# Kernel tuning notes

Hardware: AMD Instinct MI355X
Metric: run time of the kernel (lower is better)

The kernel has to match this reference:

```python
import jax, jax.numpy as jnp
import numpy as np

BATCH = 16384
NUM_CLASSES = 1000
FEA_DIM = 1024
MARGIN = 5.0


def setup_inputs() -> dict:
    key = jax.random.key(0)
    k1, k2, k3 = jax.random.split(key, 3)
    x = jax.random.normal(k1, (BATCH, FEA_DIM), dtype=jnp.float32)
    labels = jax.random.randint(k2, (BATCH,), 0, NUM_CLASSES)
    centers = jax.random.normal(k3, (NUM_CLASSES, FEA_DIM), dtype=jnp.float32)
    return {"x": x, "labels": labels, "centers": centers}


def reference(x, labels, centers):
    # Half squared euclidean distances via the GEMM expansion:
    # 0.5*||a-b||^2 = 0.5*(||a||^2 + ||b||^2 - 2 a.b)
    B = x.shape[0]
    C = centers.shape[0]
    x2 = jnp.sum(x * x, axis=1, keepdims=True)          # [B,1]
    c2 = jnp.sum(centers * centers, axis=1)             # [C]
    d_xc = 0.5 * (x2 + c2[None, :] - 2.0 * (x @ centers.T))   # [B,C]
    d_cc = 0.5 * (c2[:, None] + c2[None, :] - 2.0 * (centers @ centers.T))  # [C,C]

    is_label = labels[:, None] == jnp.arange(C)[None, :]  # [B,C] bool
    inf = jnp.float32(jnp.inf)

    # pos_center: distance to own class center
    pos = jnp.take_along_axis(d_xc, labels[:, None], axis=1)[:, 0]       # [B]
    # neg_center: min distance to any other class center
    neg = jnp.min(jnp.where(is_label, inf, d_xc), axis=1)                # [B]
    # centers term: min distance between own center and any other center
    cen = jnp.min(jnp.where(is_label, inf, d_cc[labels]), axis=1)        # [B]

    loss = jax.nn.relu(pos + MARGIN - neg) + jax.nn.relu(MARGIN + 2.0 - cen)
    return jnp.sum(loss) / B
```

## Files before the change

kernel.cpp:

```cpp
#include <hip/hip_runtime.h>
#include <hip/hip_bf16.h>
#include <stdint.h>

#define BATCH   16384
#define NCLASS  1000
#define CPAD    1024
#define FDIM    1024
#define MARGINF 5.0f

typedef __attribute__((ext_vector_type(4))) float f32x4;
typedef __attribute__((ext_vector_type(8))) short bf16x8;

__device__ __forceinline__ void gload16(const void* g, void* l) {
    __builtin_amdgcn_global_load_lds(
        (const __attribute__((address_space(1))) void*)g,
        (__attribute__((address_space(3))) void*)l, 16, 0, 0);
}

__device__ __forceinline__ unsigned short f2bf(float f) {
    __hip_bfloat16 h = __float2bfloat16(f);
    return __builtin_bit_cast(unsigned short, h);
}

__global__ void prep(const float* __restrict__ x, const float* __restrict__ c,
                     unsigned short* __restrict__ xb, unsigned short* __restrict__ cb,
                     float* __restrict__ c2) {
    const int bid = blockIdx.x;
    const int t   = threadIdx.x;
    if (bid < CPAD) {
        const int k = bid;
        if (k >= NCLASS) {
            ((ushort4*)(cb + (size_t)k * FDIM))[t] = make_ushort4(0, 0, 0, 0);
            if (t == 0) c2[k] = 1e30f;
            return;
        }
        float4 v = ((const float4*)(c + (size_t)k * FDIM))[t];
        ushort4 o;
        o.x = f2bf(v.x); o.y = f2bf(v.y); o.z = f2bf(v.z); o.w = f2bf(v.w);
        ((ushort4*)(cb + (size_t)k * FDIM))[t] = o;
        float ss = v.x * v.x + v.y * v.y + v.z * v.z + v.w * v.w;
        #pragma unroll
        for (int s = 1; s < 64; s <<= 1) ss += __shfl_xor(ss, s, 64);
        __shared__ float sred[4];
        int lane = t & 63, wid = t >> 6;
        if (lane == 0) sred[wid] = ss;
        __syncthreads();
        if (t == 0) c2[k] = sred[0] + sred[1] + sred[2] + sred[3];
    } else {
        int i = (bid - CPAD) * 256 + t;
        const int stride = 2048 * 256;
        #pragma unroll
        for (int it = 0; it < 8; ++it, i += stride) {
            float4 v = ((const float4*)x)[i];
            ushort4 o;
            o.x = f2bf(v.x); o.y = f2bf(v.y); o.z = f2bf(v.z); o.w = f2bf(v.w);
            ((ushort4*)xb)[i] = o;
        }
    }
}

__launch_bounds__(256)
__global__ void gemm_min(const unsigned short* __restrict__ xb,
                         const unsigned short* __restrict__ cb,
                         const float* __restrict__ c2,
                         const int* __restrict__ labels,
                         float* __restrict__ pmin,
                         float* __restrict__ cpmin,
                         float* __restrict__ pos,
                         float* __restrict__ out)
{
    constexpr int BM = 128, BK = 64, KTOT = 1024, NCT = 8;
    __shared__ __align__(16) char sA[BM * BK * 2];
    __shared__ __align__(16) char sB[BM * BK * 2];

    const int bid  = blockIdx.x;
    const int t    = threadIdx.x;
    if (bid == 0 && t == 0) out[0] = 0.0f;

    const bool cc  = (bid >= 1024);
    const int bx   = cc ? (bid - 1024) & 7 : bid & 127;
    const int by   = cc ? (bid - 1024) >> 3 : bid >> 7;

    const int lane = t & 63;
    const int wave = t >> 6;
    const int wrow = wave >> 1, wcol = wave & 1;
    const int lo4  = lane & 15, hi2 = lane >> 4;

    const int rowBase = bx * BM;
    const int colBase = by * BM;
    const unsigned short* A = cc ? cb : xb;
    float* pout = cc ? cpmin : pmin;

    f32x4 acc[4][4];
    #pragma unroll
    for (int m = 0; m < 4; m++)
        #pragma unroll
        for (int n = 0; n < 4; n++) acc[m][n] = (f32x4){0.f, 0.f, 0.f, 0.f};

    const int g_t = t & 7;
    const int r_t = t >> 3;

    const unsigned short* ga[4]; const unsigned short* gb[4];
    char* la[4]; char* lb[4];
    #pragma unroll
    for (int cch = 0; cch < 4; ++cch) {
        const int row = cch * 32 + r_t;
        const int sc  = g_t ^ (row & 7);
        ga[cch] = A  + (size_t)(rowBase + row) * KTOT + sc * 8;
        gb[cch] = cb + (size_t)(colBase + row) * KTOT + sc * 8;
        la[cch] = sA + (cch * 256 + (t & 192)) * 16;
        lb[cch] = sB + (cch * 256 + (t & 192)) * 16;
    }

    for (int kt = 0; kt < KTOT / BK; ++kt) {
        __syncthreads();
        #pragma unroll
        for (int cch = 0; cch < 4; ++cch) {
            gload16(ga[cch], la[cch]);
            gload16(gb[cch], lb[cch]);
            ga[cch] += BK; gb[cch] += BK;
        }
        __syncthreads();
        #pragma unroll
        for (int ks = 0; ks < 2; ++ks) {
            bf16x8 af[4], bfr[4];
            #pragma unroll
            for (int m = 0; m < 4; m++) {
                const int r    = wrow * 64 + m * 16 + lo4;
                const int slot = (ks * 4 + hi2) ^ (r & 7);
                af[m] = *(const bf16x8*)(sA + r * 128 + slot * 16);
            }
            #pragma unroll
            for (int n = 0; n < 4; n++) {
                const int r    = wcol * 64 + n * 16 + lo4;
                const int slot = (ks * 4 + hi2) ^ (r & 7);
                bfr[n] = *(const bf16x8*)(sB + r * 128 + slot * 16);
            }
            #pragma unroll
            for (int m = 0; m < 4; m++)
                #pragma unroll
                for (int n = 0; n < 4; n++)
                    acc[m][n] = __builtin_amdgcn_mfma_f32_16x16x32_bf16(af[m], bfr[n], acc[m][n], 0, 0, 0);
        }
    }

    __syncthreads();
    float* sPM = (float*)sA;

    float bias[4]; int colg[4];
    #pragma unroll
    for (int n = 0; n < 4; n++) {
        const int col = colBase + wcol * 64 + n * 16 + lo4;
        colg[n] = col;
        bias[n] = 0.5f * c2[col];
    }
    #pragma unroll
    for (int m = 0; m < 4; m++) {
        #pragma unroll
        for (int j = 0; j < 4; j++) {
            const int rloc  = wrow * 64 + m * 16 + hi2 * 4 + j;
            const int rglob = rowBase + rloc;
            const int lab   = cc ? rglob : labels[rglob];
            float vmin = 1e30f;
            #pragma unroll
            for (int n = 0; n < 4; n++) {
                float tv = acc[m][n][j] + bias[n];
                if (colg[n] == lab) {
                    if (!cc) pos[rglob] = tv;
                    tv = 1e30f;
                }
                vmin = fminf(vmin, tv);
            }
            vmin = fminf(vmin, __shfl_xor(vmin, 1, 64));
            vmin = fminf(vmin, __shfl_xor(vmin, 2, 64));
            vmin = fminf(vmin, __shfl_xor(vmin, 4, 64));
            vmin = fminf(vmin, __shfl_xor(vmin, 8, 64));
            if (lo4 == 0) sPM[wcol * BM + rloc] = vmin;
        }
    }
    __syncthreads();
    if (t < BM) {
        const float v = fminf(sPM[t], sPM[BM + t]);
        pout[(size_t)(rowBase + t) * NCT + by] = v;
    }
}

__global__ void loss_k(const float* __restrict__ pmin, const float* __restrict__ pos,
                       const int* __restrict__ labels, const float* __restrict__ cpmin,
                       const float* __restrict__ c2, float* __restrict__ out) {
    const int r = blockIdx.x * 256 + threadIdx.x;
    float neg = 1e30f;
    #pragma unroll
    for (int i = 0; i < 8; i++) neg = fminf(neg, pmin[(size_t)r * 8 + i]);
    const int lab = labels[r];
    float cmin = 1e30f;
    #pragma unroll
    for (int i = 0; i < 8; i++) cmin = fminf(cmin, cpmin[(size_t)lab * 8 + i]);
    const float cen = 0.5f * c2[lab] + cmin;
    float v = fmaxf(pos[r] + MARGINF - neg, 0.f) + fmaxf(MARGINF + 2.0f - cen, 0.f);
    #pragma unroll
    for (int s = 1; s < 64; s <<= 1) v += __shfl_xor(v, s, 64);
    __shared__ float sred[4];
    int lane = threadIdx.x & 63, wid = threadIdx.x >> 6;
    if (lane == 0) sred[wid] = v;
    __syncthreads();
    if (threadIdx.x == 0)
        atomicAdd(out, (sred[0] + sred[1] + sred[2] + sred[3]) * (1.0f / (float)BATCH));
}

extern "C" void kernel_launch(void* const* d_in, const int* in_sizes, int n_in,
                              void* d_out, int out_size, void* d_ws, size_t ws_size,
                              hipStream_t stream) {
    const float* x       = (const float*)d_in[0];
    const int*   labels  = (const int*)d_in[1];
    const float* centers = (const float*)d_in[2];
    float* out = (float*)d_out;

    char* ws = (char*)d_ws;
    size_t off = 0;
    unsigned short* xb = (unsigned short*)(ws + off); off += (size_t)BATCH * FDIM * 2;
    unsigned short* cb = (unsigned short*)(ws + off); off += (size_t)CPAD * FDIM * 2;
    float* c2    = (float*)(ws + off); off += (size_t)CPAD * 4;
    float* pmin  = (float*)(ws + off); off += (size_t)BATCH * 8 * 4;
    float* pos   = (float*)(ws + off); off += (size_t)BATCH * 4;
    float* cpmin = (float*)(ws + off); off += (size_t)CPAD * 8 * 4;

    prep<<<dim3(CPAD + 2048), dim3(256), 0, stream>>>(x, centers, xb, cb, c2);
    gemm_min<<<dim3(1024 + 64), dim3(256), 0, stream>>>(xb, cb, c2, labels, pmin, cpmin, pos, out);
    loss_k<<<dim3(BATCH / 256), dim3(256), 0, stream>>>(pmin, pos, labels, cpmin, c2, out);
}
```

Measured before the change: 168.4 us.

## Fuse prep, GEMM-min and loss into one cooperative persistent kernel

Replaces the three launches with a single cooperative kernel that uses grid-wide syncs between phases: center conversion, then x conversion overlapped with the center-center GEMM, then the x-center GEMM tiles in a persistent loop, then the loss reduction. It targets launch gaps and inter-kernel tails, and runs the small cc GEMM alongside the x conversion. The costs are grid.sync overhead, a grid capped at occupancy times CU count (up to 1024 blocks), and a loss phase where only 16 threads per block work. If the cooperative launch fails, it falls back to the old three-kernel path.

```diff
diff --git a/kernel.cpp b/kernel.cpp
--- a/kernel.cpp
+++ b/kernel.cpp
@@ -1,6 +1,9 @@
 #include <hip/hip_runtime.h>
 #include <hip/hip_bf16.h>
+#include <hip/hip_cooperative_groups.h>
 #include <stdint.h>
+
+namespace cg = cooperative_groups;
 
 #define BATCH   16384
 #define NCLASS  1000
@@ -22,11 +25,202 @@
     return __builtin_bit_cast(unsigned short, h);
 }
 
+template <bool CC>
+__device__ __forceinline__ void gemm_tile(const unsigned short* __restrict__ A,
+                                          const unsigned short* __restrict__ B,
+                                          const float* __restrict__ c2,
+                                          const int* __restrict__ labels,
+                                          float* __restrict__ pout,
+                                          float* __restrict__ pos,
+                                          int bx, int by, char* sA, char* sB)
+{
+    constexpr int BM = 128, BK = 64, KTOT = 1024, NCT = 8;
+    const int t    = threadIdx.x;
+    const int lane = t & 63;
+    const int wave = t >> 6;
+    const int wrow = wave >> 1, wcol = wave & 1;
+    const int lo4  = lane & 15, hi2 = lane >> 4;
+    const int rowBase = bx * BM;
+    const int colBase = by * BM;
+
+    f32x4 acc[4][4];
+    #pragma unroll
+    for (int m = 0; m < 4; m++)
+        #pragma unroll
+        for (int n = 0; n < 4; n++) acc[m][n] = (f32x4){0.f, 0.f, 0.f, 0.f};
+
+    const int g_t = t & 7;
+    const int r_t = t >> 3;
+
+    const unsigned short* ga[4]; const unsigned short* gb[4];
+    char* la[4]; char* lb[4];
+    #pragma unroll
+    for (int cch = 0; cch < 4; ++cch) {
+        const int row = cch * 32 + r_t;
+        const int sc  = g_t ^ (row & 7);
+        ga[cch] = A + (size_t)(rowBase + row) * KTOT + sc * 8;
+        gb[cch] = B + (size_t)(colBase + row) * KTOT + sc * 8;
+        la[cch] = sA + (cch * 256 + (t & 192)) * 16;
+        lb[cch] = sB + (cch * 256 + (t & 192)) * 16;
+    }
+
+    for (int kt = 0; kt < KTOT / BK; ++kt) {
+        __syncthreads();
+        #pragma unroll
+        for (int cch = 0; cch < 4; ++cch) {
+            gload16(ga[cch], la[cch]);
+            gload16(gb[cch], lb[cch]);
+            ga[cch] += BK; gb[cch] += BK;
+        }
+        __syncthreads();
+        #pragma unroll
+        for (int ks = 0; ks < 2; ++ks) {
+            bf16x8 af[4], bfr[4];
+            #pragma unroll
+            for (int m = 0; m < 4; m++) {
+                const int r    = wrow * 64 + m * 16 + lo4;
+                const int slot = (ks * 4 + hi2) ^ (r & 7);
+                af[m] = *(const bf16x8*)(sA + r * 128 + slot * 16);
+            }
+            #pragma unroll
+            for (int n = 0; n < 4; n++) {
+                const int r    = wcol * 64 + n * 16 + lo4;
+                const int slot = (ks * 4 + hi2) ^ (r & 7);
+                bfr[n] = *(const bf16x8*)(sB + r * 128 + slot * 16);
+            }
+            #pragma unroll
+            for (int m = 0; m < 4; m++)
+                #pragma unroll
+                for (int n = 0; n < 4; n++)
+                    acc[m][n] = __builtin_amdgcn_mfma_f32_16x16x32_bf16(af[m], bfr[n], acc[m][n], 0, 0, 0);
+        }
+    }
+
+    __syncthreads();
+    float* sPM = (float*)sA;
+
+    float bias[4]; int colg[4];
+    #pragma unroll
+    for (int n = 0; n < 4; n++) {
+        const int col = colBase + wcol * 64 + n * 16 + lo4;
+        colg[n] = col;
+        bias[n] = 0.5f * c2[col];
+    }
+    #pragma unroll
+    for (int m = 0; m < 4; m++) {
+        #pragma unroll
+        for (int j = 0; j < 4; j++) {
+            const int rloc  = wrow * 64 + m * 16 + hi2 * 4 + j;
+            const int rglob = rowBase + rloc;
+            const int lab   = CC ? rglob : labels[rglob];
+            float vmin = 1e30f;
+            #pragma unroll
+            for (int n = 0; n < 4; n++) {
+                float tv = acc[m][n][j] + bias[n];
+                if (colg[n] == lab) {
+                    if (!CC) pos[rglob] = tv;
+                    tv = 1e30f;
+                }
+                vmin = fminf(vmin, tv);
+            }
+            vmin = fminf(vmin, __shfl_xor(vmin, 1, 64));
+            vmin = fminf(vmin, __shfl_xor(vmin, 2, 64));
+            vmin = fminf(vmin, __shfl_xor(vmin, 4, 64));
+            vmin = fminf(vmin, __shfl_xor(vmin, 8, 64));
+            if (lo4 == 0) sPM[wcol * BM + rloc] = vmin;
+        }
+    }
+    __syncthreads();
+    if (t < BM) {
+        const float v = fminf(sPM[t], sPM[BM + t]);
+        pout[(size_t)(rowBase + t) * NCT + by] = v;
+    }
+    __syncthreads();
+}
+
+__launch_bounds__(256, 4)
+__global__ void mega(const float* __restrict__ x, const int* __restrict__ labels,
+                     const float* __restrict__ centers,
+                     unsigned short* xb, unsigned short* cb,
+                     float* c2, float* pmin, float* cpmin, float* pos,
+                     float* out)
+{
+    __shared__ __align__(16) char sA[128 * 64 * 2];
+    __shared__ __align__(16) char sB[128 * 64 * 2];
+
+    cg::grid_group grid = cg::this_grid();
+    const int bid = blockIdx.x;
+    const int t   = threadIdx.x;
+    const int G   = gridDim.x;
+
+    for (int k = bid; k < CPAD; k += G) {
+        if (k >= NCLASS) {
+            ((ushort4*)(cb + (size_t)k * FDIM))[t] = make_ushort4(0, 0, 0, 0);
+            if (t == 0) c2[k] = 1e30f;
+        } else {
+            float4 v = ((const float4*)(centers + (size_t)k * FDIM))[t];
+            ushort4 o;
+            o.x = f2bf(v.x); o.y = f2bf(v.y); o.z = f2bf(v.z); o.w = f2bf(v.w);
+            ((ushort4*)(cb + (size_t)k * FDIM))[t] = o;
+            float ss = v.x * v.x + v.y * v.y + v.z * v.z + v.w * v.w;
+            #pragma unroll
+            for (int s = 1; s < 64; s <<= 1) ss += __shfl_xor(ss, s, 64);
+            float* sred = (float*)sB;
+            if ((t & 63) == 0) sred[t >> 6] = ss;
+            __syncthreads();
+            if (t == 0) c2[k] = sred[0] + sred[1] + sred[2] + sred[3];
+            __syncthreads();
+        }
+    }
+    if (bid == 0 && t == 0) atomicExch(out, 0.0f);
+    grid.sync();
+
+    const int xBlocks = G - 64;
+    if (bid < xBlocks) {
+        const int n4 = BATCH * FDIM / 4;
+        for (int i = bid * 256 + t; i < n4; i += xBlocks * 256) {
+            float4 v = ((const float4*)x)[i];
+            ushort4 o;
+            o.x = f2bf(v.x); o.y = f2bf(v.y); o.z = f2bf(v.z); o.w = f2bf(v.w);
+            ((ushort4*)xb)[i] = o;
+        }
+    } else {
+        const int tile = bid - xBlocks;
+        gemm_tile<true>(cb, cb, c2, labels, cpmin, nullptr, tile & 7, tile >> 3, sA, sB);
+    }
+    grid.sync();
+
+    for (int tile = bid; tile < 1024; tile += G)
+        gemm_tile<false>(xb, cb, c2, labels, pmin, pos, tile & 127, tile >> 7, sA, sB);
+    grid.sync();
+
+    if (t < 16) {
+        float lsum = 0.f;
+        for (int r = bid * 16 + t; r < BATCH; r += G * 16) {
+            float neg = 1e30f;
+            #pragma unroll
+            for (int i = 0; i < 8; i++) neg = fminf(neg, pmin[(size_t)r * 8 + i]);
+            const int lab = labels[r];
+            float cmin = 1e30f;
+            #pragma unroll
+            for (int i = 0; i < 8; i++) cmin = fminf(cmin, cpmin[(size_t)lab * 8 + i]);
+            const float cen = 0.5f * c2[lab] + cmin;
+            lsum += fmaxf(pos[r] + MARGINF - neg, 0.f) + fmaxf(MARGINF + 2.0f - cen, 0.f);
+        }
+        lsum += __shfl_xor(lsum, 1, 64);
+        lsum += __shfl_xor(lsum, 2, 64);
+        lsum += __shfl_xor(lsum, 4, 64);
+        lsum += __shfl_xor(lsum, 8, 64);
+        if (t == 0) atomicAdd(out, lsum * (1.0f / (float)BATCH));
+    }
+}
+
 __global__ void prep(const float* __restrict__ x, const float* __restrict__ c,
                      unsigned short* __restrict__ xb, unsigned short* __restrict__ cb,
-                     float* __restrict__ c2) {
+                     float* __restrict__ c2, float* __restrict__ out) {
     const int bid = blockIdx.x;
     const int t   = threadIdx.x;
+    if (bid == 0 && t == 0) atomicExch(out, 0.0f);
     if (bid < CPAD) {
         const int k = bid;
         if (k >= NCLASS) {
@@ -64,124 +258,17 @@
                          const unsigned short* __restrict__ cb,
                          const float* __restrict__ c2,
                          const int* __restrict__ labels,
-                         float* __restrict__ pmin,
-                         float* __restrict__ cpmin,
-                         float* __restrict__ pos,
-                         float* __restrict__ out)
+                         float* __restrict__ pmin, float* __restrict__ cpmin,
+                         float* __restrict__ pos)
 {
-    constexpr int BM = 128, BK = 64, KTOT = 1024, NCT = 8;
-    __shared__ __align__(16) char sA[BM * BK * 2];
-    __shared__ __align__(16) char sB[BM * BK * 2];
-
-    const int bid  = blockIdx.x;
-    const int t    = threadIdx.x;
-    if (bid == 0 && t == 0) out[0] = 0.0f;
-
-    const bool cc  = (bid >= 1024);
-    const int bx   = cc ? (bid - 1024) & 7 : bid & 127;
-    const int by   = cc ? (bid - 1024) >> 3 : bid >> 7;
-
-    const int lane = t & 63;
-    const int wave = t >> 6;
-    const int wrow = wave >> 1, wcol = wave & 1;
-    const int lo4  = lane & 15, hi2 = lane >> 4;
-
-    const int rowBase = bx * BM;
-    const int colBase = by * BM;
-    const unsigned short* A = cc ? cb : xb;
-    float* pout = cc ? cpmin : pmin;
-
-    f32x4 acc[4][4];
-    #pragma unroll
-    for (int m = 0; m < 4; m++)
-        #pragma unroll
-        for (int n = 0; n < 4; n++) acc[m][n] = (f32x4){0.f, 0.f, 0.f, 0.f};
-
-    const int g_t = t & 7;
-    const int r_t = t >> 3;
-
-    const unsigned short* ga[4]; const unsigned short* gb[4];
-    char* la[4]; char* lb[4];
-    #pragma unroll
-    for (int cch = 0; cch < 4; ++cch) {
-        const int row = cch * 32 + r_t;
-        const int sc  = g_t ^ (row & 7);
-        ga[cch] = A  + (size_t)(rowBase + row) * KTOT + sc * 8;
-        gb[cch] = cb + (size_t)(colBase + row) * KTOT + sc * 8;
-        la[cch] = sA + (cch * 256 + (t & 192)) * 16;
-        lb[cch] = sB + (cch * 256 + (t & 192)) * 16;
-    }
-
-    for (int kt = 0; kt < KTOT / BK; ++kt) {
-        __syncthreads();
-        #pragma unroll
-        for (int cch = 0; cch < 4; ++cch) {
-            gload16(ga[cch], la[cch]);
-            gload16(gb[cch], lb[cch]);
-            ga[cch] += BK; gb[cch] += BK;
-        }
-        __syncthreads();
-        #pragma unroll
-        for (int ks = 0; ks < 2; ++ks) {
-            bf16x8 af[4], bfr[4];
-            #pragma unroll
-            for (int m = 0; m < 4; m++) {
-                const int r    = wrow * 64 + m * 16 + lo4;
-                const int slot = (ks * 4 + hi2) ^ (r & 7);
-                af[m] = *(const bf16x8*)(sA + r * 128 + slot * 16);
-            }
-            #pragma unroll
-            for (int n = 0; n < 4; n++) {
-                const int r    = wcol * 64 + n * 16 + lo4;
-                const int slot = (ks * 4 + hi2) ^ (r & 7);
-                bfr[n] = *(const bf16x8*)(sB + r * 128 + slot * 16);
-            }
-            #pragma unroll
-            for (int m = 0; m < 4; m++)
-                #pragma unroll
-                for (int n = 0; n < 4; n++)
-                    acc[m][n] = __builtin_amdgcn_mfma_f32_16x16x32_bf16(af[m], bfr[n], acc[m][n], 0, 0, 0);
-        }
-    }
-
-    __syncthreads();
-    float* sPM = (float*)sA;
-
-    float bias[4]; int colg[4];
-    #pragma unroll
-    for (int n = 0; n < 4; n++) {
-        const int col = colBase + wcol * 64 + n * 16 + lo4;
-        colg[n] = col;
-        bias[n] = 0.5f * c2[col];
-    }
-    #pragma unroll
-    for (int m = 0; m < 4; m++) {
-        #pragma unroll
-        for (int j = 0; j < 4; j++) {
-            const int rloc  = wrow * 64 + m * 16 + hi2 * 4 + j;
-            const int rglob = rowBase + rloc;
-            const int lab   = cc ? rglob : labels[rglob];
-            float vmin = 1e30f;
-            #pragma unroll
-            for (int n = 0; n < 4; n++) {
-                float tv = acc[m][n][j] + bias[n];
-                if (colg[n] == lab) {
-                    if (!cc) pos[rglob] = tv;
-                    tv = 1e30f;
-                }
-                vmin = fminf(vmin, tv);
-            }
-            vmin = fminf(vmin, __shfl_xor(vmin, 1, 64));
-            vmin = fminf(vmin, __shfl_xor(vmin, 2, 64));
-            vmin = fminf(vmin, __shfl_xor(vmin, 4, 64));
-            vmin = fminf(vmin, __shfl_xor(vmin, 8, 64));
-            if (lo4 == 0) sPM[wcol * BM + rloc] = vmin;
-        }
-    }
-    __syncthreads();
-    if (t < BM) {
-        const float v = fminf(sPM[t], sPM[BM + t]);
-        pout[(size_t)(rowBase + t) * NCT + by] = v;
+    __shared__ __align__(16) char sA[128 * 64 * 2];
+    __shared__ __align__(16) char sB[128 * 64 * 2];
+    const int bid = blockIdx.x;
+    if (bid >= 1024) {
+        const int tile = bid - 1024;
+        gemm_tile<true>(cb, cb, c2, labels, cpmin, nullptr, tile & 7, tile >> 3, sA, sB);
+    } else {
+        gemm_tile<false>(xb, cb, c2, labels, pmin, pos, bid & 127, bid >> 7, sA, sB);
     }
 }
 
@@ -225,7 +312,21 @@
     float* pos   = (float*)(ws + off); off += (size_t)BATCH * 4;
     float* cpmin = (float*)(ws + off); off += (size_t)CPAD * 8 * 4;
 
-    prep<<<dim3(CPAD + 2048), dim3(256), 0, stream>>>(x, centers, xb, cb, c2);
-    gemm_min<<<dim3(1024 + 64), dim3(256), 0, stream>>>(xb, cb, c2, labels, pmin, cpmin, pos, out);
-    loss_k<<<dim3(BATCH / 256), dim3(256), 0, stream>>>(pmin, pos, labels, cpmin, c2, out);
-}
+    int G = 1024;
+    int cus = 0, nb = 0, dev = 0;
+    (void)hipGetDevice(&dev);
+    if (hipDeviceGetAttribute(&cus, hipDeviceAttributeMultiprocessorCount, dev) == hipSuccess && cus > 0 &&
+        hipOccupancyMaxActiveBlocksPerMultiprocessor(&nb, mega, 256, 0) == hipSuccess && nb > 0) {
+        G = nb * cus;
+        if (G > 1024) G = 1024;
+    }
+
+    void* args[] = {(void*)&x, (void*)&labels, (void*)&centers, (void*)&xb, (void*)&cb,
+                    (void*)&c2, (void*)&pmin, (void*)&cpmin, (void*)&pos, (void*)&out};
+    hipError_t e = hipLaunchCooperativeKernel((void*)mega, dim3(G), dim3(256), args, 0, stream);
+    if (e != hipSuccess) {
+        prep<<<dim3(CPAD + 2048), dim3(256), 0, stream>>>(x, centers, xb, cb, c2, out);
+        gemm_min<<<dim3(1024 + 64), dim3(256), 0, stream>>>(xb, cb, c2, labels, pmin, cpmin, pos);
+        loss_k<<<dim3(BATCH / 256), dim3(256), 0, stream>>>(pmin, pos, labels, cpmin, c2, out);
+    }
+}
```

Result: slower. 388.5 us (+130.6%).

## Split center GEMM out and use 256x256 double-buffered pipelined MFMA kernel

Applied to the files above, without the earlier changes.

Moves the center-to-center distance GEMM into its own small kernel. The main batch-by-center GEMM becomes a 512-thread kernel with 256x256 tiles and a double-buffered 128KB LDS pipeline. Global-to-LDS loads for the next K slab are interleaved with MFMA bursts, using explicit waitcnt and barriers plus setprio around the MFMAs. Blocks are remapped for locality, and the output is zeroed in prep. The aim is more reuse per tile and hiding load latency, at the cost of a grid of only 256 large blocks and fragile hand-written synchronisation.

```diff
diff --git a/kernel.cpp b/kernel.cpp
--- a/kernel.cpp
+++ b/kernel.cpp
@@ -11,6 +11,12 @@
 typedef __attribute__((ext_vector_type(4))) float f32x4;
 typedef __attribute__((ext_vector_type(8))) short bf16x8;
 
+#define SB()    __builtin_amdgcn_s_barrier()
+#define LGKM0() asm volatile("s_waitcnt lgkmcnt(0)" ::: "memory")
+#define VMC4()  asm volatile("s_waitcnt vmcnt(4)" ::: "memory")
+#define VMC0()  asm volatile("s_waitcnt vmcnt(0)" ::: "memory")
+#define SCH0()  __builtin_amdgcn_sched_barrier(0)
+
 __device__ __forceinline__ void gload16(const void* g, void* l) {
     __builtin_amdgcn_global_load_lds(
         (const __attribute__((address_space(1))) void*)g,
@@ -24,9 +30,10 @@
 
 __global__ void prep(const float* __restrict__ x, const float* __restrict__ c,
                      unsigned short* __restrict__ xb, unsigned short* __restrict__ cb,
-                     float* __restrict__ c2) {
+                     float* __restrict__ c2, float* __restrict__ out) {
     const int bid = blockIdx.x;
     const int t   = threadIdx.x;
+    if (bid == 0 && t == 0) atomicExch(out, 0.0f);
     if (bid < CPAD) {
         const int k = bid;
         if (k >= NCLASS) {
@@ -60,36 +67,20 @@
 }
 
 __launch_bounds__(256)
-__global__ void gemm_min(const unsigned short* __restrict__ xb,
-                         const unsigned short* __restrict__ cb,
-                         const float* __restrict__ c2,
-                         const int* __restrict__ labels,
-                         float* __restrict__ pmin,
-                         float* __restrict__ cpmin,
-                         float* __restrict__ pos,
-                         float* __restrict__ out)
+__global__ void cc_gemm(const unsigned short* __restrict__ cb,
+                        const float* __restrict__ c2,
+                        float* __restrict__ cpmin)
 {
-    constexpr int BM = 128, BK = 64, KTOT = 1024, NCT = 8;
-    __shared__ __align__(16) char sA[BM * BK * 2];
-    __shared__ __align__(16) char sB[BM * BK * 2];
-
-    const int bid  = blockIdx.x;
+    __shared__ __align__(16) char sA[128 * 64 * 2];
+    __shared__ __align__(16) char sB[128 * 64 * 2];
+    const int bid = blockIdx.x;
+    const int bx = bid & 7, by = bid >> 3;
     const int t    = threadIdx.x;
-    if (bid == 0 && t == 0) out[0] = 0.0f;
-
-    const bool cc  = (bid >= 1024);
-    const int bx   = cc ? (bid - 1024) & 7 : bid & 127;
-    const int by   = cc ? (bid - 1024) >> 3 : bid >> 7;
-
     const int lane = t & 63;
     const int wave = t >> 6;
     const int wrow = wave >> 1, wcol = wave & 1;
     const int lo4  = lane & 15, hi2 = lane >> 4;
-
-    const int rowBase = bx * BM;
-    const int colBase = by * BM;
-    const unsigned short* A = cc ? cb : xb;
-    float* pout = cc ? cpmin : pmin;
+    const int rowBase = bx * 128, colBase = by * 128;
 
     f32x4 acc[4][4];
     #pragma unroll
@@ -97,28 +88,25 @@
         #pragma unroll
         for (int n = 0; n < 4; n++) acc[m][n] = (f32x4){0.f, 0.f, 0.f, 0.f};
 
-    const int g_t = t & 7;
-    const int r_t = t >> 3;
-
+    const int g_t = t & 7, r_t = t >> 3;
     const unsigned short* ga[4]; const unsigned short* gb[4];
     char* la[4]; char* lb[4];
     #pragma unroll
     for (int cch = 0; cch < 4; ++cch) {
         const int row = cch * 32 + r_t;
         const int sc  = g_t ^ (row & 7);
-        ga[cch] = A  + (size_t)(rowBase + row) * KTOT + sc * 8;
-        gb[cch] = cb + (size_t)(colBase + row) * KTOT + sc * 8;
+        ga[cch] = cb + (size_t)(rowBase + row) * FDIM + sc * 8;
+        gb[cch] = cb + (size_t)(colBase + row) * FDIM + sc * 8;
         la[cch] = sA + (cch * 256 + (t & 192)) * 16;
         lb[cch] = sB + (cch * 256 + (t & 192)) * 16;
     }
-
-    for (int kt = 0; kt < KTOT / BK; ++kt) {
+    for (int kt = 0; kt < 16; ++kt) {
         __syncthreads();
         #pragma unroll
         for (int cch = 0; cch < 4; ++cch) {
             gload16(ga[cch], la[cch]);
             gload16(gb[cch], lb[cch]);
-            ga[cch] += BK; gb[cch] += BK;
+            ga[cch] += 64; gb[cch] += 64;
         }
         __syncthreads();
         #pragma unroll
@@ -126,13 +114,13 @@
             bf16x8 af[4], bfr[4];
             #pragma unroll
             for (int m = 0; m < 4; m++) {
-                const int r    = wrow * 64 + m * 16 + lo4;
+                const int r = wrow * 64 + m * 16 + lo4;
                 const int slot = (ks * 4 + hi2) ^ (r & 7);
                 af[m] = *(const bf16x8*)(sA + r * 128 + slot * 16);
             }
             #pragma unroll
             for (int n = 0; n < 4; n++) {
-                const int r    = wcol * 64 + n * 16 + lo4;
+                const int r = wcol * 64 + n * 16 + lo4;
                 const int slot = (ks * 4 + hi2) ^ (r & 7);
                 bfr[n] = *(const bf16x8*)(sB + r * 128 + slot * 16);
             }
@@ -143,10 +131,8 @@
                     acc[m][n] = __builtin_amdgcn_mfma_f32_16x16x32_bf16(af[m], bfr[n], acc[m][n], 0, 0, 0);
         }
     }
-
     __syncthreads();
     float* sPM = (float*)sA;
-
     float bias[4]; int colg[4];
     #pragma unroll
     for (int n = 0; n < 4; n++) {
@@ -160,13 +146,176 @@
         for (int j = 0; j < 4; j++) {
             const int rloc  = wrow * 64 + m * 16 + hi2 * 4 + j;
             const int rglob = rowBase + rloc;
-            const int lab   = cc ? rglob : labels[rglob];
+            float vmin = 1e30f;
+            #pragma unroll
+            for (int n = 0; n < 4; n++) {
+                float tv = acc[m][n][j] + bias[n];
+                if (colg[n] == rglob) tv = 1e30f;
+                vmin = fminf(vmin, tv);
+            }
+            vmin = fminf(vmin, __shfl_xor(vmin, 1, 64));
+            vmin = fminf(vmin, __shfl_xor(vmin, 2, 64));
+            vmin = fminf(vmin, __shfl_xor(vmin, 4, 64));
+            vmin = fminf(vmin, __shfl_xor(vmin, 8, 64));
+            if (lo4 == 0) sPM[wcol * 128 + rloc] = vmin;
+        }
+    }
+    __syncthreads();
+    if (t < 128)
+        cpmin[(size_t)(rowBase + t) * 8 + by] = fminf(sPM[t], sPM[128 + t]);
+}
+
+__launch_bounds__(512, 2)
+__global__ void gemm8(const unsigned short* __restrict__ xb,
+                      const unsigned short* __restrict__ cb,
+                      const float* __restrict__ c2,
+                      const int* __restrict__ labels,
+                      float* __restrict__ pmin,
+                      float* __restrict__ pos)
+{
+    __shared__ __align__(16) char L[131072];
+
+    const int bid = blockIdx.x;
+    const int tid = (bid & 7) * 32 + (bid >> 3);
+    const int bx = tid >> 2, by = tid & 3;
+    const int rowBase = bx * 256, colBase = by * 256;
+
+    const int t    = threadIdx.x;
+    const int lane = t & 63;
+    const int w    = t >> 6;
+    const int wrow = w >> 2, wcol = w & 3;
+    const int lo4  = lane & 15, hi2 = lane >> 4;
+    const int wb   = w << 10;
+
+    const int srow = t >> 2;
+    const int g0   = (t & 3) ^ (srow & 3);
+    const unsigned short* sApt[2];
+    const unsigned short* sBpt[2];
+    sApt[0] = xb + (size_t)(rowBase + srow)       * FDIM + g0 * 8;
+    sApt[1] = xb + (size_t)(rowBase + 128 + srow) * FDIM + g0 * 8;
+    sBpt[0] = cb + (size_t)(colBase + srow)       * FDIM + g0 * 8;
+    sBpt[1] = cb + (size_t)(colBase + 128 + srow) * FDIM + g0 * 8;
+
+    auto stage = [&](int ldsOff, const unsigned short* s0, const unsigned short* s1) {
+        gload16(s0, L + ldsOff + wb);
+        gload16(s1, L + ldsOff + 8192 + wb);
+    };
+
+    const int gsw = ((hi2 ^ (lo4 & 3)) << 4);
+    auto LDA = [&](int slot, int ks, int m) -> bf16x8 {
+        const int r = wrow * 128 + m * 16 + lo4;
+        return *(const bf16x8*)(L + slot + ks * 16384 + r * 64 + gsw);
+    };
+    auto LDB = [&](int slot, int ks, int n) -> bf16x8 {
+        const int r = wcol * 64 + n * 16 + lo4;
+        return *(const bf16x8*)(L + slot + 32768 + ks * 16384 + r * 64 + gsw);
+    };
+
+    f32x4 acc[8][4];
+    #pragma unroll
+    for (int m = 0; m < 8; m++)
+        #pragma unroll
+        for (int n = 0; n < 4; n++) acc[m][n] = (f32x4){0.f, 0.f, 0.f, 0.f};
+
+    bf16x8 af[8], b0, b1;
+
+#define MFMA16(N0, N1, B0_, B1_)                                                   \
+    __builtin_amdgcn_s_setprio(1);                                                 \
+    _Pragma("unroll")                                                              \
+    for (int m = 0; m < 8; ++m) {                                                  \
+        acc[m][N0] = __builtin_amdgcn_mfma_f32_16x16x32_bf16(af[m], B0_, acc[m][N0], 0, 0, 0); \
+        acc[m][N1] = __builtin_amdgcn_mfma_f32_16x16x32_bf16(af[m], B1_, acc[m][N1], 0, 0, 0); \
+    }                                                                              \
+    __builtin_amdgcn_s_setprio(0);
+
+    stage(0,         sApt[0],      sApt[1]);
+    stage(32768,     sBpt[0],      sBpt[1]);
+    stage(16384,     sApt[0] + 32, sApt[1] + 32);
+    stage(49152,     sBpt[0] + 32, sBpt[1] + 32);
+    VMC0();
+    SB();
+
+    for (int kt = 0; kt < 15; ++kt) {
+        const int slot  = (kt & 1) << 16;
+        const int nslot = slot ^ 65536;
+        const int nk = (kt + 1) * 64;
+        #pragma unroll
+        for (int m = 0; m < 8; ++m) af[m] = LDA(slot, 0, m);
+        b0 = LDB(slot, 0, 0); b1 = LDB(slot, 0, 1);
+        stage(nslot, sApt[0] + nk, sApt[1] + nk);
+        SB(); LGKM0(); SCH0();
+        MFMA16(0, 1, b0, b1);
+        SB();
+        b0 = LDB(slot, 0, 2); b1 = LDB(slot, 0, 3);
+        stage(nslot + 32768, sBpt[0] + nk, sBpt[1] + nk);
+        SB(); LGKM0(); SCH0();
+        MFMA16(2, 3, b0, b1);
+        VMC4();
+        SB();
+        #pragma unroll
+        for (int m = 0; m < 8; ++m) af[m] = LDA(slot, 1, m);
+        b0 = LDB(slot, 1, 0); b1 = LDB(slot, 1, 1);
+        stage(nslot + 16384, sApt[0] + nk + 32, sApt[1] + nk + 32);
+        SB(); LGKM0(); SCH0();
+        MFMA16(0, 1, b0, b1);
+        SB();
+        b0 = LDB(slot, 1, 2); b1 = LDB(slot, 1, 3);
+        stage(nslot + 49152, sBpt[0] + nk + 32, sBpt[1] + nk + 32);
+        SB(); LGKM0(); SCH0();
+        MFMA16(2, 3, b0, b1);
+        VMC4();
+        SB();
+    }
+    {
+        const int slot = 65536;
+        #pragma unroll
+        for (int m = 0; m < 8; ++m) af[m] = LDA(slot, 0, m);
+        b0 = LDB(slot, 0, 0); b1 = LDB(slot, 0, 1);
+        SB(); LGKM0(); SCH0();
+        MFMA16(0, 1, b0, b1);
+        SB();
+        b0 = LDB(slot, 0, 2); b1 = LDB(slot, 0, 3);
+        SB(); LGKM0(); SCH0();
+        MFMA16(2, 3, b0, b1);
+        VMC0();
+        SB();
+        #pragma unroll
+        for (int m = 0; m < 8; ++m) af[m] = LDA(slot, 1, m);
+        b0 = LDB(slot, 1, 0); b1 = LDB(slot, 1, 1);
+        SB(); LGKM0(); SCH0();
+        MFMA16(0, 1, b0, b1);
+        SB();
+        b0 = LDB(slot, 1, 2); b1 = LDB(slot, 1, 3);
+        SB(); LGKM0(); SCH0();
+        MFMA16(2, 3, b0, b1);
+        SB();
+    }
+
+    float* sPM  = (float*)L;
+    int*   sLab = (int*)(L + 4096);
+    if (t < 256) sLab[t] = labels[rowBase + t];
+    __syncthreads();
+
+    float bias[4]; int colg[4];
+    #pragma unroll
+    for (int n = 0; n < 4; n++) {
+        const int col = colBase + wcol * 64 + n * 16 + lo4;
+        colg[n] = col;
+        bias[n] = 0.5f * c2[col];
+    }
+    #pragma unroll
+    for (int m = 0; m < 8; m++) {
+        #pragma unroll
+        for (int j = 0; j < 4; j++) {
+            const int rloc  = wrow * 128 + m * 16 + hi2 * 4 + j;
+            const int rglob = rowBase + rloc;
+            const int lab   = sLab[rloc];
             float vmin = 1e30f;
             #pragma unroll
             for (int n = 0; n < 4; n++) {
                 float tv = acc[m][n][j] + bias[n];
                 if (colg[n] == lab) {
-                    if (!cc) pos[rglob] = tv;
+                    pos[rglob] = tv;
                     tv = 1e30f;
                 }
                 vmin = fminf(vmin, tv);
@@ -175,14 +324,15 @@
             vmin = fminf(vmin, __shfl_xor(vmin, 2, 64));
             vmin = fminf(vmin, __shfl_xor(vmin, 4, 64));
             vmin = fminf(vmin, __shfl_xor(vmin, 8, 64));
-            if (lo4 == 0) sPM[wcol * BM + rloc] = vmin;
-        }
-    }
-    __syncthreads();
-    if (t < BM) {
-        const float v = fminf(sPM[t], sPM[BM + t]);
-        pout[(size_t)(rowBase + t) * NCT + by] = v;
-    }
+            if (lo4 == 0) sPM[wcol * 256 + rloc] = vmin;
+        }
+    }
+    __syncthreads();
+    if (t < 256) {
+        const float v = fminf(fminf(sPM[t], sPM[256 + t]), fminf(sPM[512 + t], sPM[768 + t]));
+        pmin[(size_t)(rowBase + t) * 4 + by] = v;
+    }
+#undef MFMA16
 }
 
 __global__ void loss_k(const float* __restrict__ pmin, const float* __restrict__ pos,
@@ -191,7 +341,7 @@
     const int r = blockIdx.x * 256 + threadIdx.x;
     float neg = 1e30f;
     #pragma unroll
-    for (int i = 0; i < 8; i++) neg = fminf(neg, pmin[(size_t)r * 8 + i]);
+    for (int i = 0; i < 4; i++) neg = fminf(neg, pmin[(size_t)r * 4 + i]);
     const int lab = labels[r];
     float cmin = 1e30f;
     #pragma unroll
@@ -221,11 +371,12 @@
     unsigned short* xb = (unsigned short*)(ws + off); off += (size_t)BATCH * FDIM * 2;
     unsigned short* cb = (unsigned short*)(ws + off); off += (size_t)CPAD * FDIM * 2;
     float* c2    = (float*)(ws + off); off += (size_t)CPAD * 4;
-    float* pmin  = (float*)(ws + off); off += (size_t)BATCH * 8 * 4;
+    float* pmin  = (float*)(ws + off); off += (size_t)BATCH * 4 * 4;
     float* pos   = (float*)(ws + off); off += (size_t)BATCH * 4;
     float* cpmin = (float*)(ws + off); off += (size_t)CPAD * 8 * 4;
 
-    prep<<<dim3(CPAD + 2048), dim3(256), 0, stream>>>(x, centers, xb, cb, c2);
-    gemm_min<<<dim3(1024 + 64), dim3(256), 0, stream>>>(xb, cb, c2, labels, pmin, cpmin, pos, out);
+    prep<<<dim3(CPAD + 2048), dim3(256), 0, stream>>>(x, centers, xb, cb, c2, out);
+    cc_gemm<<<dim3(64), dim3(256), 0, stream>>>(cb, c2, cpmin);
+    gemm8<<<dim3(256), dim3(512), 0, stream>>>(xb, cb, c2, labels, pmin, pos);
     loss_k<<<dim3(BATCH / 256), dim3(256), 0, stream>>>(pmin, pos, labels, cpmin, c2, out);
 }
```

After: 163.6 us. 2.9% less time.
